# Kernel optimization log

Hardware: AMD Instinct MI355X
Metric: run time of the kernel (lower is better)

Reference implementation:

```python
import jax, jax.numpy as jnp
import numpy as np

EMB = 256
ENT_NUM = 100000
REL_NUM = 2000
B = 512


def setup_inputs() -> dict:
    key = jax.random.key(0)
    ks = jax.random.split(key, 10)
    s = 0.02
    return {
        "left_child": jax.random.normal(ks[0], (B, 3, EMB), jnp.float32),
        "right_child": jax.random.normal(ks[1], (B, 3, EMB), jnp.float32),
        "query": jax.random.normal(ks[2], (B, 3, EMB), jnp.float32),
        "ent_emb": jax.random.normal(ks[3], (ENT_NUM, EMB), jnp.float32) * s,
        "rel_emb": jax.random.normal(ks[4], (REL_NUM, EMB), jnp.float32) * s,
        "W_left": jax.random.normal(ks[5], (EMB, EMB), jnp.float32) * s,
        "b_left": jnp.zeros((EMB,), jnp.float32),
        "W_right": jax.random.normal(ks[6], (EMB, EMB), jnp.float32) * s,
        "b_right": jnp.zeros((EMB,), jnp.float32),
        "W_ent": jax.random.normal(ks[7], (EMB, 3 * EMB), jnp.float32) * s,
        "b_ent": jnp.zeros((EMB,), jnp.float32),
    }


def _attend(q, table):
    # q: [B, E], table: [N, E]. Fused form of expand*mul*sum + softmax + expand*mul*sum.
    logits = q @ table.T                     # [B, N]
    probs = jax.nn.softmax(logits, axis=1)   # [B, N]
    return probs @ table                     # [B, E]


def reference(left_child, right_child, query, ent_emb, rel_emb,
              W_left, b_left, W_right, b_right, W_ent, b_ent):
    q1 = query[:, 1, :]
    left_rel = q1 @ W_left.T + b_left
    right_rel = q1 @ W_right.T + b_right
    # cat(query[:,0], query[:,1], query[:,2]) along dim 1 == reshape
    q_cat = query.reshape(query.shape[0], 3 * EMB)
    q_ent = q_cat @ W_ent.T + b_ent

    o_ent = _attend(q_ent, ent_emb)
    o_left_r = _attend(left_rel, rel_emb)
    o_right_r = _attend(right_rel, rel_emb)

    new_left = jnp.stack([left_child[:, 0, :], o_left_r, o_ent], axis=1)
    new_right = jnp.stack([o_ent, o_right_r, right_child[:, 2, :]], axis=1)
    return (new_left, new_right)
```

## Files before the change

kernel.cpp:

```cpp
#include <hip/hip_runtime.h>
#include <hip/hip_bf16.h>
#include <math.h>

typedef __bf16 bf16;
typedef unsigned short u16;
typedef unsigned int u32;
typedef unsigned long long u64;
typedef long long i64;
typedef unsigned char u8;
typedef __attribute__((ext_vector_type(8))) __bf16 bf16x8;
typedef __attribute__((ext_vector_type(16))) float f32x16;
typedef __attribute__((ext_vector_type(8))) int i32x8;
typedef __attribute__((address_space(1))) void gvoid;
typedef __attribute__((address_space(3))) void svoid;

#define ENT_N 100000
#define REL_N 2000
#define ENT_CH 120
#define REL_CH 4

#define NPREPM 1536
#define NITEMS 6380
#define NCOPY  256

static __device__ __forceinline__ i32x8 mk8(uint4 a, uint4 b) {
    i32x8 r;
    r[0] = (int)a.x; r[1] = (int)a.y; r[2] = (int)a.z; r[3] = (int)a.w;
    r[4] = (int)b.x; r[5] = (int)b.y; r[6] = (int)b.z; r[7] = (int)b.w;
    return r;
}

template<int KLEN>
static __device__ __forceinline__ void prep_tile(
    const float* __restrict__ query, const float* __restrict__ W,
    const float* __restrict__ bias, int b0, int rowbase, int qwoff,
    bf16* __restrict__ outBf, u8* __restrict__ out8, float* smem)
{
    const int t = threadIdx.x;
    float* qs = smem;
    float* Wl = smem + 4 * KLEN;

#pragma unroll
    for (int i = 0; i < 4 * KLEN / 256; ++i) {
        const int l = t + 256 * i;
        const int r = l / KLEN, k = l % KLEN;
        qs[l] = query[(size_t)(b0 + r) * 768 + qwoff + k];
    }

    const int j = t & 63, r = t >> 6;
    const int srow = t >> 3, skq = t & 7;
    const float* wbase = W + (size_t)rowbase * KLEN;

    float4 v0, v1;
    auto wload = [&](int c) {
        v0 = *(const float4*)(wbase + (size_t)srow * KLEN + c * 32 + skq * 4);
        v1 = *(const float4*)(wbase + (size_t)(srow + 32) * KLEN + c * 32 + skq * 4);
    };
    auto wstore = [&](float* dst) {
        float* d0 = dst + srow * 33 + skq * 4;
        d0[0] = v0.x; d0[1] = v0.y; d0[2] = v0.z; d0[3] = v0.w;
        float* d1 = dst + (srow + 32) * 33 + skq * 4;
        d1[0] = v1.x; d1[1] = v1.y; d1[2] = v1.z; d1[3] = v1.w;
    };

    float acc = 0.f;
    wload(0);
    wstore(Wl);
    constexpr int NC = KLEN / 32;
    for (int c = 0; c < NC; ++c) {
        if (c + 1 < NC) wload(c + 1);
        __syncthreads();
        const float* wr = Wl + (c & 1) * 2112 + j * 33;
        const float* qr = qs + r * KLEN + c * 32;
#pragma unroll
        for (int k = 0; k < 32; ++k) acc += wr[k] * qr[k];
        if (c + 1 < NC) wstore(Wl + ((c + 1) & 1) * 2112);
    }
    acc += bias[rowbase + j];

    const size_t o = (size_t)(b0 + r) * 256 + rowbase + j;
    outBf[o] = (bf16)acc;
    out8[o] = (u8)__builtin_amdgcn_cvt_pk_fp8_f32(acc, acc, 0, false);
}

__global__ __launch_bounds__(256) void prep_conv(
    const float* __restrict__ query,
    const float* __restrict__ W_left, const float* __restrict__ b_left,
    const float* __restrict__ W_right, const float* __restrict__ b_right,
    const float* __restrict__ W_ent, const float* __restrict__ b_ent,
    const float* __restrict__ lc, const float* __restrict__ rc,
    bf16* __restrict__ qe, bf16* __restrict__ ql, bf16* __restrict__ qr,
    u8* __restrict__ qe8, u8* __restrict__ ql8, u8* __restrict__ qr8,
    float* __restrict__ out,
    const float* __restrict__ entF, const float* __restrict__ relF,
    u8* __restrict__ entT, u8* __restrict__ entB,
    u8* __restrict__ relT, u8* __restrict__ relB,
    int nconv)
{
    __shared__ float smem[7296];
    const int blk = blockIdx.x;
    const int t = threadIdx.x;

    if (blk < NPREPM) {
        const int rg = blk / 12, jt = blk % 12;
        const int b0 = rg * 4;
        const int proj = jt >> 2, rowbase = (jt & 3) * 64;
        if (proj == 0)
            prep_tile<768>(query, W_ent, b_ent, b0, rowbase, 0, qe, qe8, smem);
        else if (proj == 1)
            prep_tile<256>(query, W_left, b_left, b0, rowbase, 256, ql, ql8, smem);
        else
            prep_tile<256>(query, W_right, b_right, b0, rowbase, 256, qr, qr8, smem);
        return;
    }
    if (blk >= NPREPM + nconv) {
        const int idx = (blk - NPREPM - nconv) * 256 + t;
        if (idx < 32768) {
            const int q = idx >> 6, e4 = idx & 63;
            float4 v = *(const float4*)(lc + (size_t)q * 768 + e4 * 4);
            *(float4*)(out + (size_t)q * 768 + e4 * 4) = v;
        } else {
            const int j = idx - 32768;
            const int q = j >> 6, e4 = j & 63;
            float4 v = *(const float4*)(rc + (size_t)q * 768 + 512 + e4 * 4);
            *(float4*)(out + (size_t)393216 + q * 768 + 512 + e4 * 4) = v;
        }
        return;
    }

    const int cidx = blk - NPREPM;
    const int x = cidx >> 2, y = cidx & 3;
    const float* in; u8* outT; u8* outB; int R; int g;
    if (x < 1563) {
        in = entF; outT = entT; outB = entB; R = ENT_N; g = x;
    } else {
        in = relF; outT = relT; outB = relB; R = REL_N; g = x - 1563;
    }
    const int r0 = g * 64;
    float* tile = smem;
    const int e0 = y * 64;

    const int eg = t & 7, rowb = t >> 3;
#pragma unroll
    for (int item = 0; item < 2; ++item) {
        const int r = rowb + item * 32;
        float4 a, b;
        if ((r0 + r) < R) {
            const float* src = in + (size_t)(r0 + r) * 256 + e0 + eg * 8;
            a = *(const float4*)src;
            b = *(const float4*)(src + 4);
        } else { a = make_float4(0.f, 0.f, 0.f, 0.f); b = a; }
        float* dst = tile + r * 65 + eg * 8;
        dst[0] = a.x; dst[1] = a.y; dst[2] = a.z; dst[3] = a.w;
        dst[4] = b.x; dst[5] = b.y; dst[6] = b.z; dst[7] = b.w;
    }
    __syncthreads();

    {
        const int n2 = t >> 2, piece = t & 3;
        const int sub = n2 >> 5, nn = n2 & 31;
        const int kbk = piece >> 1, jh = piece & 1;
        const float* src = tile + n2 * 65 + kbk * 32 + jh * 16;
        u32 xx; uint4 o;
        xx = __builtin_amdgcn_cvt_pk_fp8_f32(src[0], src[1], 0, false);
        o.x = __builtin_amdgcn_cvt_pk_fp8_f32(src[2], src[3], xx, true);
        xx = __builtin_amdgcn_cvt_pk_fp8_f32(src[4], src[5], 0, false);
        o.y = __builtin_amdgcn_cvt_pk_fp8_f32(src[6], src[7], xx, true);
        xx = __builtin_amdgcn_cvt_pk_fp8_f32(src[8], src[9], 0, false);
        o.z = __builtin_amdgcn_cvt_pk_fp8_f32(src[10], src[11], xx, true);
        xx = __builtin_amdgcn_cvt_pk_fp8_f32(src[12], src[13], 0, false);
        o.w = __builtin_amdgcn_cvt_pk_fp8_f32(src[14], src[15], xx, true);
        *(uint4*)(outB + (size_t)g * 16384 + sub * 8192 +
                  (size_t)y * 2048 + kbk * 1024 + nn * 32 + jh * 16) = o;
    }
    {
        const int etl = t >> 7, kbv = (t >> 6) & 1;
        const int nv = (t >> 1) & 31, jh = t & 1;
        const int colL = etl * 32 + nv;
        float v[16];
#pragma unroll
        for (int i = 0; i < 16; ++i) {
            const int row = jh * 32 + (i & 3) + 8 * (i >> 2) + 4 * kbv;
            v[i] = tile[row * 65 + colL];
        }
        u32 xx; uint4 o;
        xx = __builtin_amdgcn_cvt_pk_fp8_f32(v[0], v[1], 0, false);
        o.x = __builtin_amdgcn_cvt_pk_fp8_f32(v[2], v[3], xx, true);
        xx = __builtin_amdgcn_cvt_pk_fp8_f32(v[4], v[5], 0, false);
        o.y = __builtin_amdgcn_cvt_pk_fp8_f32(v[6], v[7], xx, true);
        xx = __builtin_amdgcn_cvt_pk_fp8_f32(v[8], v[9], 0, false);
        o.z = __builtin_amdgcn_cvt_pk_fp8_f32(v[10], v[11], xx, true);
        xx = __builtin_amdgcn_cvt_pk_fp8_f32(v[12], v[13], 0, false);
        o.w = __builtin_amdgcn_cvt_pk_fp8_f32(v[14], v[15], xx, true);
        *(uint4*)(outT + (size_t)g * 16384 +
                  (size_t)(y * 2 + etl) * 2048 +
                  kbv * 1024 + nv * 32 + jh * 16) = o;
    }
}

__global__ __launch_bounds__(256, 2) void flash10(
    const u8* __restrict__ qeP, const u8* __restrict__ qlP,
    const u8* __restrict__ qrP,
    const u8* __restrict__ entB, const u8* __restrict__ relB,
    const u8* __restrict__ entT, const u8* __restrict__ relT,
    float* __restrict__ entL, float* __restrict__ relLL,
    float* __restrict__ relLR,
    u16* __restrict__ entO, u16* __restrict__ relOL, u16* __restrict__ relOR)
{
    const int tid = threadIdx.x;
    const int w = tid >> 6;
    const int lane = tid & 63;
    const int n = lane & 31;
    const int kb = lane >> 5;

    int qt, c, stride, nt, Nrows;
    const u8* qbf; const u8* tabB; const u8* tabT;
    float* pL; u16* pO;
    {
        const int id = blockIdx.x;
        if (id < 480) {
            qt = id / 120; c = id % 120;
            stride = 120; nt = (c < 3) ? 14 : 13;
            Nrows = ENT_N;
            qbf = qeP; tabB = entB; tabT = entT; pL = entL; pO = entO;
        } else {
            const int r = id - 480;
            qt = (r >> 2) & 3; c = r & 3;
            stride = 4; nt = 8;
            Nrows = REL_N;
            tabB = relB; tabT = relT;
            if (r < 16) { qbf = qlP; pL = relLL; pO = relOL; }
            else        { qbf = qrP; pL = relLR; pO = relOR; }
        }
    }
    const int q0 = qt * 128;
    const int qw = q0 + w * 32;

    __shared__ __align__(16) u8 lds[65536];
    u16* lds16 = (u16*)lds;

    const u8* qrow = qbf + (size_t)(qw + n) * 256;
    i32x8 qf[4];
#pragma unroll
    for (int kc = 0; kc < 4; ++kc) {
        uint4 a = *(const uint4*)(qrow + kc * 64 + kb * 32);
        uint4 b = *(const uint4*)(qrow + kc * 64 + kb * 32 + 16);
        qf[kc] = mk8(a, b);
    }

    f32x16 acc[8];
#pragma unroll
    for (int et = 0; et < 8; ++et)
#pragma unroll
        for (int i = 0; i < 16; ++i) acc[et][i] = 0.f;
    float l_run = 0.f;

    auto stage = [&](int buf, int g) {
        u8* sK = lds + buf * 32768;
        u8* sV = sK + 16384;
        const u8* ksrc = tabB + (size_t)g * 16384 + w * 4096 + (size_t)lane * 16;
        const u8* vsrc = tabT + (size_t)g * 16384 + w * 4096 + (size_t)lane * 16;
#pragma unroll
        for (int o = 0; o < 4096; o += 1024) {
            __builtin_amdgcn_global_load_lds((gvoid*)(ksrc + o),
                                             (svoid*)(sK + w * 4096 + o), 16, 0, 0);
            __builtin_amdgcn_global_load_lds((gvoid*)(vsrc + o),
                                             (svoid*)(sV + w * 4096 + o), 16, 0, 0);
        }
    };

    int rt = c;
    stage(0, rt);
    __syncthreads();

    for (int k = 0; k < nt; ++k) {
        if (k + 1 < nt) stage((k + 1) & 1, rt + stride);

        const u8* sK = lds + (k & 1) * 32768;
        const u8* sV = sK + 16384;
        const int gr = rt * 64;

        f32x16 L0, L1;
#pragma unroll
        for (int i = 0; i < 16; ++i) { L0[i] = 0.f; L1[i] = 0.f; }
        const u8* kbase = sK + kb * 1024 + n * 32;
#pragma unroll
        for (int kc = 0; kc < 4; ++kc) {
            uint4 a0 = *(const uint4*)(kbase + kc * 2048);
            uint4 a1 = *(const uint4*)(kbase + kc * 2048 + 16);
            L0 = __builtin_amdgcn_mfma_scale_f32_32x32x64_f8f6f4(
                mk8(a0, a1), qf[kc], L0, 0, 0, 0, 0x7f7f7f7f, 0, 0x7f7f7f7f);
            uint4 b0 = *(const uint4*)(kbase + 8192 + kc * 2048);
            uint4 b1 = *(const uint4*)(kbase + 8192 + kc * 2048 + 16);
            L1 = __builtin_amdgcn_mfma_scale_f32_32x32x64_f8f6f4(
                mk8(b0, b1), qf[kc], L1, 0, 0, 0, 0x7f7f7f7f, 0, 0x7f7f7f7f);
        }
        if (gr + 64 > Nrows) {
#pragma unroll
            for (int r = 0; r < 16; ++r) {
                const int row = (r & 3) + 8 * (r >> 2) + 4 * kb;
                if (gr + row >= Nrows)      L0[r] = -1e30f;
                if (gr + 32 + row >= Nrows) L1[r] = -1e30f;
            }
        }
        float rs = 0.f;
#pragma unroll
        for (int r = 0; r < 16; ++r) {
            const float p0 = __expf(L0[r]); L0[r] = p0; rs += p0;
            const float p1 = __expf(L1[r]); L1[r] = p1; rs += p1;
        }
        rs += __shfl_xor(rs, 32);
        l_run += rs;
        u32 p[8];
#pragma unroll
        for (int i = 0; i < 4; ++i) {
            u32 x = __builtin_amdgcn_cvt_pk_fp8_f32(L0[i * 4 + 0], L0[i * 4 + 1], 0, false);
            p[i] = __builtin_amdgcn_cvt_pk_fp8_f32(L0[i * 4 + 2], L0[i * 4 + 3], x, true);
            u32 y = __builtin_amdgcn_cvt_pk_fp8_f32(L1[i * 4 + 0], L1[i * 4 + 1], 0, false);
            p[i + 4] = __builtin_amdgcn_cvt_pk_fp8_f32(L1[i * 4 + 2], L1[i * 4 + 3], y, true);
        }
        uint4 pa; pa.x = p[0]; pa.y = p[1]; pa.z = p[2]; pa.w = p[3];
        uint4 pb; pb.x = p[4]; pb.y = p[5]; pb.z = p[6]; pb.w = p[7];
        const i32x8 bv = mk8(pa, pb);
        const u8* vbase = sV + kb * 1024 + n * 32;
#pragma unroll
        for (int et = 0; et < 8; ++et) {
            uint4 v0 = *(const uint4*)(vbase + et * 2048);
            uint4 v1 = *(const uint4*)(vbase + et * 2048 + 16);
            acc[et] = __builtin_amdgcn_mfma_scale_f32_32x32x64_f8f6f4(
                mk8(v0, v1), bv, acc[et], 0, 0, 0, 0x7f7f7f7f, 0, 0x7f7f7f7f);
        }
        rt += stride;
        __syncthreads();
    }

    if (lane < 32) pL[(size_t)c * 512 + qw + n] = l_run;

    for (int half = 0; half < 2; ++half) {
        __syncthreads();
        if ((w >> 1) == half) {
            u16* rgn = lds16 + (w & 1) * 8448;
#pragma unroll
            for (int et = 0; et < 8; ++et)
#pragma unroll
                for (int a2 = 0; a2 < 4; ++a2) {
                    bf16 h0 = (bf16)acc[et][a2 * 4 + 0];
                    bf16 h1 = (bf16)acc[et][a2 * 4 + 1];
                    bf16 h2 = (bf16)acc[et][a2 * 4 + 2];
                    bf16 h3 = (bf16)acc[et][a2 * 4 + 3];
                    uint2 pk;
                    pk.x = ((u32)(*(u16*)&h1) << 16) | (u32)(*(u16*)&h0);
                    pk.y = ((u32)(*(u16*)&h3) << 16) | (u32)(*(u16*)&h2);
                    *(uint2*)(rgn + n * 264 + et * 32 + 8 * a2 + 4 * kb) = pk;
                }
        }
        __syncthreads();
#pragma unroll
        for (int rg = 0; rg < 2; ++rg) {
            const int qt2 = q0 + (half * 2 + rg) * 32;
            const u16* src = lds16 + rg * 8448;
            const int qq = tid >> 3, e0 = (tid & 7) * 32;
#pragma unroll
            for (int i = 0; i < 4; ++i) {
                const u16* sp = src + qq * 264 + e0 + i * 8;
                uint2 a = *(const uint2*)(sp);
                uint2 b = *(const uint2*)(sp + 4);
                uint4 wv; wv.x = a.x; wv.y = a.y; wv.z = b.x; wv.w = b.y;
                *(uint4*)(pO + ((size_t)c * 512 + qt2 + qq) * 256 + e0 + i * 8) = wv;
            }
        }
    }
}

__global__ __launch_bounds__(256) void combine_all(
    const u16* __restrict__ entO, const float* __restrict__ entL,
    const u16* __restrict__ relOL, const float* __restrict__ relLL,
    const u16* __restrict__ relOR, const float* __restrict__ relLR,
    float* __restrict__ out)
{
    const u16* pO; const float* pl; int CH, baseA, baseB;
    if (blockIdx.y == 0) { pO = entO; pl = entL; CH = ENT_CH; baseA = 512; baseB = 393216; }
    else if (blockIdx.y == 1) { pO = relOL; pl = relLL; CH = REL_CH; baseA = 256; baseB = -1; }
    else { pO = relOR; pl = relLR; CH = REL_CH; baseA = 393472; baseB = -1; }

    const int t = threadIdx.x;
    const int qi = t >> 7;
    const int e0g = (t >> 2) & 31;
    const int seg = t & 3;
    const int q = blockIdx.x * 2 + qi;
    const int e0 = e0g * 8;
    const int cnt = CH >> 2;
    const int cbeg = seg * cnt;

    float s = 0.f;
    float a[8];
#pragma unroll
    for (int k = 0; k < 8; ++k) a[k] = 0.f;
#pragma unroll 6
    for (int c = cbeg; c < cbeg + cnt; ++c) {
        s += pl[(size_t)c * 512 + q];
        const uint4 wv = *(const uint4*)(pO + ((size_t)c * 512 + q) * 256 + e0);
        const u32 ww[4] = {wv.x, wv.y, wv.z, wv.w};
#pragma unroll
        for (int p = 0; p < 4; ++p) {
            a[p * 2]     += __uint_as_float((ww[p] & 0xffffu) << 16);
            a[p * 2 + 1] += __uint_as_float(ww[p] & 0xffff0000u);
        }
    }

    __shared__ float red[2][32][4][11];
    float* slot = red[qi][e0g][seg];
#pragma unroll
    for (int k = 0; k < 8; ++k) slot[k] = a[k];
    slot[8] = s;
    __syncthreads();
    if (seg == 0) {
        float st = 0.f;
        float b[8];
#pragma unroll
        for (int k = 0; k < 8; ++k) b[k] = 0.f;
#pragma unroll
        for (int sgi = 0; sgi < 4; ++sgi) {
            const float* sl = red[qi][e0g][sgi];
            st += sl[8];
#pragma unroll
            for (int k = 0; k < 8; ++k) b[k] += sl[k];
        }
        const float inv = 1.f / st;
#pragma unroll
        for (int k = 0; k < 8; ++k) b[k] *= inv;
        float4 o1 = {b[0], b[1], b[2], b[3]};
        float4 o2 = {b[4], b[5], b[6], b[7]};
        *(float4*)(out + (size_t)baseA + (size_t)q * 768 + e0) = o1;
        *(float4*)(out + (size_t)baseA + (size_t)q * 768 + e0 + 4) = o2;
        if (baseB >= 0) {
            *(float4*)(out + (size_t)baseB + (size_t)q * 768 + e0) = o1;
            *(float4*)(out + (size_t)baseB + (size_t)q * 768 + e0 + 4) = o2;
        }
    }
}

__global__ __launch_bounds__(256) void attend_simple(
    const bf16* __restrict__ qbf, const float* __restrict__ tab, int Nrows,
    float* __restrict__ out, int baseA, int baseB)
{
    const int q = blockIdx.x;
    const int t = threadIdx.x, wave = t >> 6, lane = t & 63;
    float qv[4];
#pragma unroll
    for (int i = 0; i < 4; ++i) qv[i] = (float)qbf[(size_t)q * 256 + lane + 64 * i];
    float m = -INFINITY, l = 0.f, o[4] = {0.f, 0.f, 0.f, 0.f};
    for (int r = wave; r < Nrows; r += 4) {
        const float* row = tab + (size_t)r * 256;
        float d = 0.f;
#pragma unroll
        for (int i = 0; i < 4; ++i) d += qv[i] * row[lane + 64 * i];
#pragma unroll
        for (int s = 32; s; s >>= 1) d += __shfl_xor(d, s);
        const float mn = fmaxf(m, d);
        const float al = __expf(m - mn);
        const float p = __expf(d - mn);
#pragma unroll
        for (int i = 0; i < 4; ++i) o[i] = o[i] * al + p * row[lane + 64 * i];
        l = l * al + p; m = mn;
    }
    __shared__ float sm[4], sl[4], so[4][256];
    if (lane == 0) { sm[wave] = m; sl[wave] = l; }
#pragma unroll
    for (int i = 0; i < 4; ++i) so[wave][lane + 64 * i] = o[i];
    __syncthreads();
    const float M = fmaxf(fmaxf(sm[0], sm[1]), fmaxf(sm[2], sm[3]));
    const float w0 = __expf(sm[0] - M), w1 = __expf(sm[1] - M);
    const float w2 = __expf(sm[2] - M), w3 = __expf(sm[3] - M);
    const float L = w0 * sl[0] + w1 * sl[1] + w2 * sl[2] + w3 * sl[3];
    const float a = (w0 * so[0][t] + w1 * so[1][t] + w2 * so[2][t] + w3 * so[3][t]) / L;
    out[(size_t)baseA + (size_t)q * 768 + t] = a;
    if (baseB >= 0) out[(size_t)baseB + (size_t)q * 768 + t] = a;
}

extern "C" void kernel_launch(void* const* d_in, const int* in_sizes, int n_in,
                              void* d_out, int out_size, void* d_ws, size_t ws_size,
                              hipStream_t stream)
{
    const float* left_child  = (const float*)d_in[0];
    const float* right_child = (const float*)d_in[1];
    const float* query       = (const float*)d_in[2];
    const float* ent_emb     = (const float*)d_in[3];
    const float* rel_emb     = (const float*)d_in[4];
    const float* W_left      = (const float*)d_in[5];
    const float* b_left      = (const float*)d_in[6];
    const float* W_right     = (const float*)d_in[7];
    const float* b_right     = (const float*)d_in[8];
    const float* W_ent       = (const float*)d_in[9];
    const float* b_ent       = (const float*)d_in[10];
    float* out = (float*)d_out;
    char* ws = (char*)d_ws;

    bf16* qe_bf = (bf16*)(ws + 0);
    bf16* ql_bf = (bf16*)(ws + 262144);
    bf16* qr_bf = (bf16*)(ws + 524288);
    u8*   qe8   = (u8*)(ws + 786432);
    u8*   ql8   = (u8*)(ws + 917504);
    u8*   qr8   = (u8*)(ws + 1048576);
    u8*   entT8 = (u8*)(ws + 1179648);
    u8*   relT8 = (u8*)(ws + 26787840);
    u8*   entB8 = (u8*)(ws + 27312128);
    u8*   relB8 = (u8*)(ws + 52920320);
    float* entL = (float*)(ws + 53444608);
    u16*  entO  = (u16*)(ws + 53690368);
    float* relLL = (float*)(ws + 85147648);
    float* relLR = (float*)(ws + 85155840);
    u16*  relOL = (u16*)(ws + 85164032);
    u16*  relOR = (u16*)(ws + 86212608);
    const size_t WS_FULL = 87261184;
    const size_t WS_FALLBACK = 786432;

    if (ws_size >= WS_FULL) {
        prep_conv<<<dim3(NPREPM + NITEMS + NCOPY), dim3(256), 0, stream>>>(
            query, W_left, b_left, W_right, b_right, W_ent, b_ent,
            left_child, right_child, qe_bf, ql_bf, qr_bf, qe8, ql8, qr8, out,
            ent_emb, rel_emb, entT8, entB8, relT8, relB8, NITEMS);
        flash10<<<dim3(512), dim3(256), 0, stream>>>(
            qe8, ql8, qr8, entB8, relB8, entT8, relT8,
            entL, relLL, relLR, entO, relOL, relOR);
        combine_all<<<dim3(256, 3), dim3(256), 0, stream>>>(
            entO, entL, relOL, relLL, relOR, relLR, out);
    } else if (ws_size >= WS_FALLBACK) {
        prep_conv<<<dim3(NPREPM + NCOPY), dim3(256), 0, stream>>>(
            query, W_left, b_left, W_right, b_right, W_ent, b_ent,
            left_child, right_child, qe_bf, ql_bf, qr_bf, qe8, ql8, qr8, out,
            ent_emb, rel_emb, (u8*)ws, (u8*)ws, (u8*)ws, (u8*)ws, 0);
        attend_simple<<<dim3(512), dim3(256), 0, stream>>>(qe_bf, ent_emb, ENT_N, out, 512, 393216);
        attend_simple<<<dim3(512), dim3(256), 0, stream>>>(ql_bf, rel_emb, REL_N, out, 256, -1);
        attend_simple<<<dim3(512), dim3(256), 0, stream>>>(qr_bf, rel_emb, REL_N, out, 393472, -1);
    }
    (void)in_sizes; (void)n_in; (void)out_size;
}
```

Before: 236.8 us.

## Coarsen fp8 conversion blocks to process four column slices with prefetch

Each conversion block now handles all four 64-column slices of a 64-row group instead of one, prefetching the next slice's global loads into registers while the current slice is converted and stored. The copy blocks each move four float4 items per thread instead of one. This cuts the grid from ~8k to ~3.2k blocks and overlaps load latency with the conversion work. In exchange it adds extra barriers per block and reduces parallelism per block count.

```diff
diff --git a/kernel.cpp b/kernel.cpp
--- a/kernel.cpp
+++ b/kernel.cpp
@@ -8,7 +8,6 @@
 typedef unsigned long long u64;
 typedef long long i64;
 typedef unsigned char u8;
-typedef __attribute__((ext_vector_type(8))) __bf16 bf16x8;
 typedef __attribute__((ext_vector_type(16))) float f32x16;
 typedef __attribute__((ext_vector_type(8))) int i32x8;
 typedef __attribute__((address_space(1))) void gvoid;
@@ -20,8 +19,8 @@
 #define REL_CH 4
 
 #define NPREPM 1536
-#define NITEMS 6380
-#define NCOPY  256
+#define NCONVG 1595
+#define NCOPYB 64
 
 static __device__ __forceinline__ i32x8 mk8(uint4 a, uint4 b) {
     i32x8 r;
@@ -114,87 +113,101 @@
         return;
     }
     if (blk >= NPREPM + nconv) {
-        const int idx = (blk - NPREPM - nconv) * 256 + t;
-        if (idx < 32768) {
-            const int q = idx >> 6, e4 = idx & 63;
-            float4 v = *(const float4*)(lc + (size_t)q * 768 + e4 * 4);
-            *(float4*)(out + (size_t)q * 768 + e4 * 4) = v;
-        } else {
-            const int j = idx - 32768;
-            const int q = j >> 6, e4 = j & 63;
-            float4 v = *(const float4*)(rc + (size_t)q * 768 + 512 + e4 * 4);
-            *(float4*)(out + (size_t)393216 + q * 768 + 512 + e4 * 4) = v;
+        const int base = (blk - NPREPM - nconv) * 256 + t;
+#pragma unroll
+        for (int i = 0; i < 4; ++i) {
+            const int idx = base + i * 16384;
+            if (idx < 32768) {
+                const int q = idx >> 6, e4 = idx & 63;
+                float4 v = *(const float4*)(lc + (size_t)q * 768 + e4 * 4);
+                *(float4*)(out + (size_t)q * 768 + e4 * 4) = v;
+            } else {
+                const int j = idx - 32768;
+                const int q = j >> 6, e4 = j & 63;
+                float4 v = *(const float4*)(rc + (size_t)q * 768 + 512 + e4 * 4);
+                *(float4*)(out + (size_t)393216 + q * 768 + 512 + e4 * 4) = v;
+            }
         }
         return;
     }
 
-    const int cidx = blk - NPREPM;
-    const int x = cidx >> 2, y = cidx & 3;
+    const int cb = blk - NPREPM;
     const float* in; u8* outT; u8* outB; int R; int g;
-    if (x < 1563) {
-        in = entF; outT = entT; outB = entB; R = ENT_N; g = x;
+    if (cb < 1563) {
+        in = entF; outT = entT; outB = entB; R = ENT_N; g = cb;
     } else {
-        in = relF; outT = relT; outB = relB; R = REL_N; g = x - 1563;
+        in = relF; outT = relT; outB = relB; R = REL_N; g = cb - 1563;
     }
     const int r0 = g * 64;
     float* tile = smem;
-    const int e0 = y * 64;
-
     const int eg = t & 7, rowb = t >> 3;
-#pragma unroll
-    for (int item = 0; item < 2; ++item) {
-        const int r = rowb + item * 32;
-        float4 a, b;
-        if ((r0 + r) < R) {
-            const float* src = in + (size_t)(r0 + r) * 256 + e0 + eg * 8;
-            a = *(const float4*)src;
-            b = *(const float4*)(src + 4);
-        } else { a = make_float4(0.f, 0.f, 0.f, 0.f); b = a; }
-        float* dst = tile + r * 65 + eg * 8;
-        dst[0] = a.x; dst[1] = a.y; dst[2] = a.z; dst[3] = a.w;
-        dst[4] = b.x; dst[5] = b.y; dst[6] = b.z; dst[7] = b.w;
-    }
-    __syncthreads();
-
-    {
-        const int n2 = t >> 2, piece = t & 3;
-        const int sub = n2 >> 5, nn = n2 & 31;
-        const int kbk = piece >> 1, jh = piece & 1;
-        const float* src = tile + n2 * 65 + kbk * 32 + jh * 16;
-        u32 xx; uint4 o;
-        xx = __builtin_amdgcn_cvt_pk_fp8_f32(src[0], src[1], 0, false);
-        o.x = __builtin_amdgcn_cvt_pk_fp8_f32(src[2], src[3], xx, true);
-        xx = __builtin_amdgcn_cvt_pk_fp8_f32(src[4], src[5], 0, false);
-        o.y = __builtin_amdgcn_cvt_pk_fp8_f32(src[6], src[7], xx, true);
-        xx = __builtin_amdgcn_cvt_pk_fp8_f32(src[8], src[9], 0, false);
-        o.z = __builtin_amdgcn_cvt_pk_fp8_f32(src[10], src[11], xx, true);
-        xx = __builtin_amdgcn_cvt_pk_fp8_f32(src[12], src[13], 0, false);
-        o.w = __builtin_amdgcn_cvt_pk_fp8_f32(src[14], src[15], xx, true);
-        *(uint4*)(outB + (size_t)g * 16384 + sub * 8192 +
-                  (size_t)y * 2048 + kbk * 1024 + nn * 32 + jh * 16) = o;
-    }
-    {
-        const int etl = t >> 7, kbv = (t >> 6) & 1;
-        const int nv = (t >> 1) & 31, jh = t & 1;
-        const int colL = etl * 32 + nv;
-        float v[16];
-#pragma unroll
-        for (int i = 0; i < 16; ++i) {
-            const int row = jh * 32 + (i & 3) + 8 * (i >> 2) + 4 * kbv;
-            v[i] = tile[row * 65 + colL];
-        }
-        u32 xx; uint4 o;
-        xx = __builtin_amdgcn_cvt_pk_fp8_f32(v[0], v[1], 0, false);
-        o.x = __builtin_amdgcn_cvt_pk_fp8_f32(v[2], v[3], xx, true);
-        xx = __builtin_amdgcn_cvt_pk_fp8_f32(v[4], v[5], 0, false);
-        o.y = __builtin_amdgcn_cvt_pk_fp8_f32(v[6], v[7], xx, true);
-        xx = __builtin_amdgcn_cvt_pk_fp8_f32(v[8], v[9], 0, false);
-        o.z = __builtin_amdgcn_cvt_pk_fp8_f32(v[10], v[11], xx, true);
-        xx = __builtin_amdgcn_cvt_pk_fp8_f32(v[12], v[13], 0, false);
-        o.w = __builtin_amdgcn_cvt_pk_fp8_f32(v[14], v[15], xx, true);
-        *(uint4*)(outT + (size_t)g * 16384 +
-                  (size_t)(y * 2 + etl) * 2048 +
-                  kbv * 1024 + nv * 32 + jh * 16) = o;
+    const bool vA = (r0 + rowb) < R, vB = (r0 + rowb + 32) < R;
+    const float* rowA = in + (size_t)(r0 + rowb) * 256 + eg * 8;
+    const float* rowB = in + (size_t)(r0 + rowb + 32) * 256 + eg * 8;
+
+    float4 A0, B0, A1, B1;
+    auto cissue = [&](int y) {
+        const int e0 = y * 64;
+        if (vA) { A0 = *(const float4*)(rowA + e0); B0 = *(const float4*)(rowA + e0 + 4); }
+        else    { A0 = make_float4(0.f, 0.f, 0.f, 0.f); B0 = A0; }
+        if (vB) { A1 = *(const float4*)(rowB + e0); B1 = *(const float4*)(rowB + e0 + 4); }
+        else    { A1 = make_float4(0.f, 0.f, 0.f, 0.f); B1 = A1; }
+    };
+
+    cissue(0);
+#pragma unroll
+    for (int y = 0; y < 4; ++y) {
+        __syncthreads();
+        {
+            float* d0 = tile + rowb * 65 + eg * 8;
+            d0[0] = A0.x; d0[1] = A0.y; d0[2] = A0.z; d0[3] = A0.w;
+            d0[4] = B0.x; d0[5] = B0.y; d0[6] = B0.z; d0[7] = B0.w;
+            float* d1 = tile + (rowb + 32) * 65 + eg * 8;
+            d1[0] = A1.x; d1[1] = A1.y; d1[2] = A1.z; d1[3] = A1.w;
+            d1[4] = B1.x; d1[5] = B1.y; d1[6] = B1.z; d1[7] = B1.w;
+        }
+        if (y + 1 < 4) cissue(y + 1);
+        __syncthreads();
+        {
+            const int n2 = t >> 2, piece = t & 3;
+            const int sub = n2 >> 5, nn = n2 & 31;
+            const int kbk = piece >> 1, jh = piece & 1;
+            const float* src = tile + n2 * 65 + kbk * 32 + jh * 16;
+            u32 xx; uint4 o;
+            xx = __builtin_amdgcn_cvt_pk_fp8_f32(src[0], src[1], 0, false);
+            o.x = __builtin_amdgcn_cvt_pk_fp8_f32(src[2], src[3], xx, true);
+            xx = __builtin_amdgcn_cvt_pk_fp8_f32(src[4], src[5], 0, false);
+            o.y = __builtin_amdgcn_cvt_pk_fp8_f32(src[6], src[7], xx, true);
+            xx = __builtin_amdgcn_cvt_pk_fp8_f32(src[8], src[9], 0, false);
+            o.z = __builtin_amdgcn_cvt_pk_fp8_f32(src[10], src[11], xx, true);
+            xx = __builtin_amdgcn_cvt_pk_fp8_f32(src[12], src[13], 0, false);
+            o.w = __builtin_amdgcn_cvt_pk_fp8_f32(src[14], src[15], xx, true);
+            *(uint4*)(outB + (size_t)g * 16384 + sub * 8192 +
+                      (size_t)y * 2048 + kbk * 1024 + nn * 32 + jh * 16) = o;
+        }
+        {
+            const int etl = t >> 7, kbv = (t >> 6) & 1;
+            const int nv = (t >> 1) & 31, jh = t & 1;
+            const int colL = etl * 32 + nv;
+            float v[16];
+#pragma unroll
+            for (int i = 0; i < 16; ++i) {
+                const int row = jh * 32 + (i & 3) + 8 * (i >> 2) + 4 * kbv;
+                v[i] = tile[row * 65 + colL];
+            }
+            u32 xx; uint4 o;
+            xx = __builtin_amdgcn_cvt_pk_fp8_f32(v[0], v[1], 0, false);
+            o.x = __builtin_amdgcn_cvt_pk_fp8_f32(v[2], v[3], xx, true);
+            xx = __builtin_amdgcn_cvt_pk_fp8_f32(v[4], v[5], 0, false);
+            o.y = __builtin_amdgcn_cvt_pk_fp8_f32(v[6], v[7], xx, true);
+            xx = __builtin_amdgcn_cvt_pk_fp8_f32(v[8], v[9], 0, false);
+            o.z = __builtin_amdgcn_cvt_pk_fp8_f32(v[10], v[11], xx, true);
+            xx = __builtin_amdgcn_cvt_pk_fp8_f32(v[12], v[13], 0, false);
+            o.w = __builtin_amdgcn_cvt_pk_fp8_f32(v[14], v[15], xx, true);
+            *(uint4*)(outT + (size_t)g * 16384 +
+                      (size_t)(y * 2 + etl) * 2048 +
+                      kbv * 1024 + nv * 32 + jh * 16) = o;
+        }
     }
 }
 
@@ -516,17 +529,17 @@
     const size_t WS_FALLBACK = 786432;
 
     if (ws_size >= WS_FULL) {
-        prep_conv<<<dim3(NPREPM + NITEMS + NCOPY), dim3(256), 0, stream>>>(
+        prep_conv<<<dim3(NPREPM + NCONVG + NCOPYB), dim3(256), 0, stream>>>(
             query, W_left, b_left, W_right, b_right, W_ent, b_ent,
             left_child, right_child, qe_bf, ql_bf, qr_bf, qe8, ql8, qr8, out,
-            ent_emb, rel_emb, entT8, entB8, relT8, relB8, NITEMS);
+            ent_emb, rel_emb, entT8, entB8, relT8, relB8, NCONVG);
         flash10<<<dim3(512), dim3(256), 0, stream>>>(
             qe8, ql8, qr8, entB8, relB8, entT8, relT8,
             entL, relLL, relLR, entO, relOL, relOR);
         combine_all<<<dim3(256, 3), dim3(256), 0, stream>>>(
             entO, entL, relOL, relLL, relOR, relLR, out);
     } else if (ws_size >= WS_FALLBACK) {
-        prep_conv<<<dim3(NPREPM + NCOPY), dim3(256), 0, stream>>>(
+        prep_conv<<<dim3(NPREPM + NCOPYB), dim3(256), 0, stream>>>(
             query, W_left, b_left, W_right, b_right, W_ent, b_ent,
             left_child, right_child, qe_bf, ql_bf, qr_bf, qe8, ql8, qr8, out,
             ent_emb, rel_emb, (u8*)ws, (u8*)ws, (u8*)ws, (u8*)ws, 0);
```

New measurement: 238.4 us. Within noise of the previous version (+0.7%).

## Fuse flash attention and combine kernels via software grid barrier

Applied to the files above, without the earlier changes.

Merges the flash-attention partial kernel and the combine kernel into one launch, separated by an atomic-counter grid barrier, with a memset added to reset the counter each call. This removes one kernel launch and the gap between kernels. It relies on all 512 blocks being co-resident (256 CUs at 2 blocks per CU) or the barrier deadlocks, and it adds a memset plus spin-wait overhead. The combine work is now spread over 512 blocks in a grid-stride loop instead of 768 blocks.

```diff
diff --git a/kernel.cpp b/kernel.cpp
--- a/kernel.cpp
+++ b/kernel.cpp
@@ -8,7 +8,6 @@
 typedef unsigned long long u64;
 typedef long long i64;
 typedef unsigned char u8;
-typedef __attribute__((ext_vector_type(8))) __bf16 bf16x8;
 typedef __attribute__((ext_vector_type(16))) float f32x16;
 typedef __attribute__((ext_vector_type(8))) int i32x8;
 typedef __attribute__((address_space(1))) void gvoid;
@@ -22,12 +21,25 @@
 #define NPREPM 1536
 #define NITEMS 6380
 #define NCOPY  256
+#define NBLK   512
 
 static __device__ __forceinline__ i32x8 mk8(uint4 a, uint4 b) {
     i32x8 r;
     r[0] = (int)a.x; r[1] = (int)a.y; r[2] = (int)a.z; r[3] = (int)a.w;
     r[4] = (int)b.x; r[5] = (int)b.y; r[6] = (int)b.z; r[7] = (int)b.w;
     return r;
+}
+
+static __device__ __forceinline__ void grid_barrier(u32* cnt) {
+    __syncthreads();
+    if (threadIdx.x == 0) {
+        __threadfence();
+        atomicAdd(cnt, 1u);
+        while (atomicAdd(cnt, 0u) < (u32)NBLK)
+            __builtin_amdgcn_s_sleep(2);
+        __threadfence();
+    }
+    __syncthreads();
 }
 
 template<int KLEN>
@@ -198,14 +210,15 @@
     }
 }
 
-__global__ __launch_bounds__(256, 2) void flash10(
+__global__ __launch_bounds__(256, 2) void flash_combine(
     const u8* __restrict__ qeP, const u8* __restrict__ qlP,
     const u8* __restrict__ qrP,
     const u8* __restrict__ entB, const u8* __restrict__ relB,
     const u8* __restrict__ entT, const u8* __restrict__ relT,
     float* __restrict__ entL, float* __restrict__ relLL,
     float* __restrict__ relLR,
-    u16* __restrict__ entO, u16* __restrict__ relOL, u16* __restrict__ relOR)
+    u16* __restrict__ entO, u16* __restrict__ relOL, u16* __restrict__ relOR,
+    float* __restrict__ out, u32* __restrict__ cnt0)
 {
     const int tid = threadIdx.x;
     const int w = tid >> 6;
@@ -213,229 +226,232 @@
     const int n = lane & 31;
     const int kb = lane >> 5;
 
-    int qt, c, stride, nt, Nrows;
-    const u8* qbf; const u8* tabB; const u8* tabT;
-    float* pL; u16* pO;
-    {
-        const int id = blockIdx.x;
-        if (id < 480) {
-            qt = id / 120; c = id % 120;
-            stride = 120; nt = (c < 3) ? 14 : 13;
-            Nrows = ENT_N;
-            qbf = qeP; tabB = entB; tabT = entT; pL = entL; pO = entO;
-        } else {
-            const int r = id - 480;
-            qt = (r >> 2) & 3; c = r & 3;
-            stride = 4; nt = 8;
-            Nrows = REL_N;
-            tabB = relB; tabT = relT;
-            if (r < 16) { qbf = qlP; pL = relLL; pO = relOL; }
-            else        { qbf = qrP; pL = relLR; pO = relOR; }
-        }
-    }
-    const int q0 = qt * 128;
-    const int qw = q0 + w * 32;
-
     __shared__ __align__(16) u8 lds[65536];
     u16* lds16 = (u16*)lds;
 
-    const u8* qrow = qbf + (size_t)(qw + n) * 256;
-    i32x8 qf[4];
-#pragma unroll
-    for (int kc = 0; kc < 4; ++kc) {
-        uint4 a = *(const uint4*)(qrow + kc * 64 + kb * 32);
-        uint4 b = *(const uint4*)(qrow + kc * 64 + kb * 32 + 16);
-        qf[kc] = mk8(a, b);
-    }
-
-    f32x16 acc[8];
-#pragma unroll
-    for (int et = 0; et < 8; ++et)
-#pragma unroll
-        for (int i = 0; i < 16; ++i) acc[et][i] = 0.f;
-    float l_run = 0.f;
-
-    auto stage = [&](int buf, int g) {
-        u8* sK = lds + buf * 32768;
-        u8* sV = sK + 16384;
-        const u8* ksrc = tabB + (size_t)g * 16384 + w * 4096 + (size_t)lane * 16;
-        const u8* vsrc = tabT + (size_t)g * 16384 + w * 4096 + (size_t)lane * 16;
-#pragma unroll
-        for (int o = 0; o < 4096; o += 1024) {
-            __builtin_amdgcn_global_load_lds((gvoid*)(ksrc + o),
-                                             (svoid*)(sK + w * 4096 + o), 16, 0, 0);
-            __builtin_amdgcn_global_load_lds((gvoid*)(vsrc + o),
-                                             (svoid*)(sV + w * 4096 + o), 16, 0, 0);
-        }
-    };
-
-    int rt = c;
-    stage(0, rt);
-    __syncthreads();
-
-    for (int k = 0; k < nt; ++k) {
-        if (k + 1 < nt) stage((k + 1) & 1, rt + stride);
-
-        const u8* sK = lds + (k & 1) * 32768;
-        const u8* sV = sK + 16384;
-        const int gr = rt * 64;
-
-        f32x16 L0, L1;
-#pragma unroll
-        for (int i = 0; i < 16; ++i) { L0[i] = 0.f; L1[i] = 0.f; }
-        const u8* kbase = sK + kb * 1024 + n * 32;
+    {
+        int qt, c, stride, nt, Nrows;
+        const u8* qbf; const u8* tabB; const u8* tabT;
+        float* pL; u16* pO;
+        {
+            const int id = blockIdx.x;
+            if (id < 480) {
+                qt = id / 120; c = id % 120;
+                stride = 120; nt = (c < 3) ? 14 : 13;
+                Nrows = ENT_N;
+                qbf = qeP; tabB = entB; tabT = entT; pL = entL; pO = entO;
+            } else {
+                const int r = id - 480;
+                qt = (r >> 2) & 3; c = r & 3;
+                stride = 4; nt = 8;
+                Nrows = REL_N;
+                tabB = relB; tabT = relT;
+                if (r < 16) { qbf = qlP; pL = relLL; pO = relOL; }
+                else        { qbf = qrP; pL = relLR; pO = relOR; }
+            }
+        }
+        const int q0 = qt * 128;
+        const int qw = q0 + w * 32;
+
+        const u8* qrow = qbf + (size_t)(qw + n) * 256;
+        i32x8 qf[4];
 #pragma unroll
         for (int kc = 0; kc < 4; ++kc) {
-            uint4 a0 = *(const uint4*)(kbase + kc * 2048);
-            uint4 a1 = *(const uint4*)(kbase + kc * 2048 + 16);
-            L0 = __builtin_amdgcn_mfma_scale_f32_32x32x64_f8f6f4(
-                mk8(a0, a1), qf[kc], L0, 0, 0, 0, 0x7f7f7f7f, 0, 0x7f7f7f7f);
-            uint4 b0 = *(const uint4*)(kbase + 8192 + kc * 2048);
-            uint4 b1 = *(const uint4*)(kbase + 8192 + kc * 2048 + 16);
-            L1 = __builtin_amdgcn_mfma_scale_f32_32x32x64_f8f6f4(
-                mk8(b0, b1), qf[kc], L1, 0, 0, 0, 0x7f7f7f7f, 0, 0x7f7f7f7f);
-        }
-        if (gr + 64 > Nrows) {
+            uint4 a = *(const uint4*)(qrow + kc * 64 + kb * 32);
+            uint4 b = *(const uint4*)(qrow + kc * 64 + kb * 32 + 16);
+            qf[kc] = mk8(a, b);
+        }
+
+        f32x16 acc[8];
+#pragma unroll
+        for (int et = 0; et < 8; ++et)
+#pragma unroll
+            for (int i = 0; i < 16; ++i) acc[et][i] = 0.f;
+        float l_run = 0.f;
+
+        auto stage = [&](int buf, int g) {
+            u8* sK = lds + buf * 32768;
+            u8* sV = sK + 16384;
+            const u8* ksrc = tabB + (size_t)g * 16384 + w * 4096 + (size_t)lane * 16;
+            const u8* vsrc = tabT + (size_t)g * 16384 + w * 4096 + (size_t)lane * 16;
+#pragma unroll
+            for (int o = 0; o < 4096; o += 1024) {
+                __builtin_amdgcn_global_load_lds((gvoid*)(ksrc + o),
+                                                 (svoid*)(sK + w * 4096 + o), 16, 0, 0);
+                __builtin_amdgcn_global_load_lds((gvoid*)(vsrc + o),
+                                                 (svoid*)(sV + w * 4096 + o), 16, 0, 0);
+            }
+        };
+
+        int rt = c;
+        stage(0, rt);
+        __syncthreads();
+
+        for (int k = 0; k < nt; ++k) {
+            if (k + 1 < nt) stage((k + 1) & 1, rt + stride);
+
+            const u8* sK = lds + (k & 1) * 32768;
+            const u8* sV = sK + 16384;
+            const int gr = rt * 64;
+
+            f32x16 L0, L1;
+#pragma unroll
+            for (int i = 0; i < 16; ++i) { L0[i] = 0.f; L1[i] = 0.f; }
+            const u8* kbase = sK + kb * 1024 + n * 32;
+#pragma unroll
+            for (int kc = 0; kc < 4; ++kc) {
+                uint4 a0 = *(const uint4*)(kbase + kc * 2048);
+                uint4 a1 = *(const uint4*)(kbase + kc * 2048 + 16);
+                L0 = __builtin_amdgcn_mfma_scale_f32_32x32x64_f8f6f4(
+                    mk8(a0, a1), qf[kc], L0, 0, 0, 0, 0x7f7f7f7f, 0, 0x7f7f7f7f);
+                uint4 b0 = *(const uint4*)(kbase + 8192 + kc * 2048);
+                uint4 b1 = *(const uint4*)(kbase + 8192 + kc * 2048 + 16);
+                L1 = __builtin_amdgcn_mfma_scale_f32_32x32x64_f8f6f4(
+                    mk8(b0, b1), qf[kc], L1, 0, 0, 0, 0x7f7f7f7f, 0, 0x7f7f7f7f);
+            }
+            if (gr + 64 > Nrows) {
+#pragma unroll
+                for (int r = 0; r < 16; ++r) {
+                    const int row = (r & 3) + 8 * (r >> 2) + 4 * kb;
+                    if (gr + row >= Nrows)      L0[r] = -1e30f;
+                    if (gr + 32 + row >= Nrows) L1[r] = -1e30f;
+                }
+            }
+            float rs = 0.f;
 #pragma unroll
             for (int r = 0; r < 16; ++r) {
-                const int row = (r & 3) + 8 * (r >> 2) + 4 * kb;
-                if (gr + row >= Nrows)      L0[r] = -1e30f;
-                if (gr + 32 + row >= Nrows) L1[r] = -1e30f;
-            }
-        }
-        float rs = 0.f;
-#pragma unroll
-        for (int r = 0; r < 16; ++r) {
-            const float p0 = __expf(L0[r]); L0[r] = p0; rs += p0;
-            const float p1 = __expf(L1[r]); L1[r] = p1; rs += p1;
-        }
-        rs += __shfl_xor(rs, 32);
-        l_run += rs;
-        u32 p[8];
-#pragma unroll
-        for (int i = 0; i < 4; ++i) {
-            u32 x = __builtin_amdgcn_cvt_pk_fp8_f32(L0[i * 4 + 0], L0[i * 4 + 1], 0, false);
-            p[i] = __builtin_amdgcn_cvt_pk_fp8_f32(L0[i * 4 + 2], L0[i * 4 + 3], x, true);
-            u32 y = __builtin_amdgcn_cvt_pk_fp8_f32(L1[i * 4 + 0], L1[i * 4 + 1], 0, false);
-            p[i + 4] = __builtin_amdgcn_cvt_pk_fp8_f32(L1[i * 4 + 2], L1[i * 4 + 3], y, true);
-        }
-        uint4 pa; pa.x = p[0]; pa.y = p[1]; pa.z = p[2]; pa.w = p[3];
-        uint4 pb; pb.x = p[4]; pb.y = p[5]; pb.z = p[6]; pb.w = p[7];
-        const i32x8 bv = mk8(pa, pb);
-        const u8* vbase = sV + kb * 1024 + n * 32;
-#pragma unroll
-        for (int et = 0; et < 8; ++et) {
-            uint4 v0 = *(const uint4*)(vbase + et * 2048);
-            uint4 v1 = *(const uint4*)(vbase + et * 2048 + 16);
-            acc[et] = __builtin_amdgcn_mfma_scale_f32_32x32x64_f8f6f4(
-                mk8(v0, v1), bv, acc[et], 0, 0, 0, 0x7f7f7f7f, 0, 0x7f7f7f7f);
-        }
-        rt += stride;
-        __syncthreads();
-    }
-
-    if (lane < 32) pL[(size_t)c * 512 + qw + n] = l_run;
-
-    for (int half = 0; half < 2; ++half) {
-        __syncthreads();
-        if ((w >> 1) == half) {
-            u16* rgn = lds16 + (w & 1) * 8448;
-#pragma unroll
-            for (int et = 0; et < 8; ++et)
-#pragma unroll
-                for (int a2 = 0; a2 < 4; ++a2) {
-                    bf16 h0 = (bf16)acc[et][a2 * 4 + 0];
-                    bf16 h1 = (bf16)acc[et][a2 * 4 + 1];
-                    bf16 h2 = (bf16)acc[et][a2 * 4 + 2];
-                    bf16 h3 = (bf16)acc[et][a2 * 4 + 3];
-                    uint2 pk;
-                    pk.x = ((u32)(*(u16*)&h1) << 16) | (u32)(*(u16*)&h0);
-                    pk.y = ((u32)(*(u16*)&h3) << 16) | (u32)(*(u16*)&h2);
-                    *(uint2*)(rgn + n * 264 + et * 32 + 8 * a2 + 4 * kb) = pk;
+                const float p0 = __expf(L0[r]); L0[r] = p0; rs += p0;
+                const float p1 = __expf(L1[r]); L1[r] = p1; rs += p1;
+            }
+            rs += __shfl_xor(rs, 32);
+            l_run += rs;
+            u32 p[8];
+#pragma unroll
+            for (int i = 0; i < 4; ++i) {
+                u32 x = __builtin_amdgcn_cvt_pk_fp8_f32(L0[i * 4 + 0], L0[i * 4 + 1], 0, false);
+                p[i] = __builtin_amdgcn_cvt_pk_fp8_f32(L0[i * 4 + 2], L0[i * 4 + 3], x, true);
+                u32 y = __builtin_amdgcn_cvt_pk_fp8_f32(L1[i * 4 + 0], L1[i * 4 + 1], 0, false);
+                p[i + 4] = __builtin_amdgcn_cvt_pk_fp8_f32(L1[i * 4 + 2], L1[i * 4 + 3], y, true);
+            }
+            uint4 pa; pa.x = p[0]; pa.y = p[1]; pa.z = p[2]; pa.w = p[3];
+            uint4 pb; pb.x = p[4]; pb.y = p[5]; pb.z = p[6]; pb.w = p[7];
+            const i32x8 bv = mk8(pa, pb);
+            const u8* vbase = sV + kb * 1024 + n * 32;
+#pragma unroll
+            for (int et = 0; et < 8; ++et) {
+                uint4 v0 = *(const uint4*)(vbase + et * 2048);
+                uint4 v1 = *(const uint4*)(vbase + et * 2048 + 16);
+                acc[et] = __builtin_amdgcn_mfma_scale_f32_32x32x64_f8f6f4(
+                    mk8(v0, v1), bv, acc[et], 0, 0, 0, 0x7f7f7f7f, 0, 0x7f7f7f7f);
+            }
+            rt += stride;
+            __syncthreads();
+        }
+
+        if (lane < 32) pL[(size_t)c * 512 + qw + n] = l_run;
+
+        for (int half = 0; half < 2; ++half) {
+            __syncthreads();
+            if ((w >> 1) == half) {
+                u16* rgn = lds16 + (w & 1) * 8448;
+#pragma unroll
+                for (int et = 0; et < 8; ++et)
+#pragma unroll
+                    for (int a2 = 0; a2 < 4; ++a2) {
+                        bf16 h0 = (bf16)acc[et][a2 * 4 + 0];
+                        bf16 h1 = (bf16)acc[et][a2 * 4 + 1];
+                        bf16 h2 = (bf16)acc[et][a2 * 4 + 2];
+                        bf16 h3 = (bf16)acc[et][a2 * 4 + 3];
+                        uint2 pk;
+                        pk.x = ((u32)(*(u16*)&h1) << 16) | (u32)(*(u16*)&h0);
+                        pk.y = ((u32)(*(u16*)&h3) << 16) | (u32)(*(u16*)&h2);
+                        *(uint2*)(rgn + n * 264 + et * 32 + 8 * a2 + 4 * kb) = pk;
+                    }
+            }
+            __syncthreads();
+#pragma unroll
+            for (int rg = 0; rg < 2; ++rg) {
+                const int qt2 = q0 + (half * 2 + rg) * 32;
+                const u16* src = lds16 + rg * 8448;
+                const int qq = tid >> 3, e0 = (tid & 7) * 32;
+#pragma unroll
+                for (int i = 0; i < 4; ++i) {
+                    const u16* sp = src + qq * 264 + e0 + i * 8;
+                    uint2 a = *(const uint2*)(sp);
+                    uint2 b = *(const uint2*)(sp + 4);
+                    uint4 wv; wv.x = a.x; wv.y = a.y; wv.z = b.x; wv.w = b.y;
+                    *(uint4*)(pO + ((size_t)c * 512 + qt2 + qq) * 256 + e0 + i * 8) = wv;
                 }
-        }
-        __syncthreads();
-#pragma unroll
-        for (int rg = 0; rg < 2; ++rg) {
-            const int qt2 = q0 + (half * 2 + rg) * 32;
-            const u16* src = lds16 + rg * 8448;
-            const int qq = tid >> 3, e0 = (tid & 7) * 32;
-#pragma unroll
-            for (int i = 0; i < 4; ++i) {
-                const u16* sp = src + qq * 264 + e0 + i * 8;
-                uint2 a = *(const uint2*)(sp);
-                uint2 b = *(const uint2*)(sp + 4);
-                uint4 wv; wv.x = a.x; wv.y = a.y; wv.z = b.x; wv.w = b.y;
-                *(uint4*)(pO + ((size_t)c * 512 + qt2 + qq) * 256 + e0 + i * 8) = wv;
-            }
-        }
-    }
-}
-
-__global__ __launch_bounds__(256) void combine_all(
-    const u16* __restrict__ entO, const float* __restrict__ entL,
-    const u16* __restrict__ relOL, const float* __restrict__ relLL,
-    const u16* __restrict__ relOR, const float* __restrict__ relLR,
-    float* __restrict__ out)
-{
-    const u16* pO; const float* pl; int CH, baseA, baseB;
-    if (blockIdx.y == 0) { pO = entO; pl = entL; CH = ENT_CH; baseA = 512; baseB = 393216; }
-    else if (blockIdx.y == 1) { pO = relOL; pl = relLL; CH = REL_CH; baseA = 256; baseB = -1; }
-    else { pO = relOR; pl = relLR; CH = REL_CH; baseA = 393472; baseB = -1; }
-
-    const int t = threadIdx.x;
-    const int qi = t >> 7;
-    const int e0g = (t >> 2) & 31;
-    const int seg = t & 3;
-    const int q = blockIdx.x * 2 + qi;
-    const int e0 = e0g * 8;
-    const int cnt = CH >> 2;
-    const int cbeg = seg * cnt;
-
-    float s = 0.f;
-    float a[8];
-#pragma unroll
-    for (int k = 0; k < 8; ++k) a[k] = 0.f;
+            }
+        }
+    }
+    grid_barrier(cnt0);
+
+    {
+        const int t = threadIdx.x;
+        typedef float RedT[32][4][11];
+        RedT* red = (RedT*)lds;
+        for (int v = blockIdx.x; v < 768; v += NBLK) {
+            __syncthreads();
+            const int gx = v & 255, gy = v >> 8;
+            const u16* pO; const float* pl; int CH, baseA, baseB;
+            if (gy == 0) { pO = entO; pl = entL; CH = ENT_CH; baseA = 512; baseB = 393216; }
+            else if (gy == 1) { pO = relOL; pl = relLL; CH = REL_CH; baseA = 256; baseB = -1; }
+            else { pO = relOR; pl = relLR; CH = REL_CH; baseA = 393472; baseB = -1; }
+
+            const int qi = t >> 7;
+            const int e0g = (t >> 2) & 31;
+            const int seg = t & 3;
+            const int q = gx * 2 + qi;
+            const int e0 = e0g * 8;
+            const int cnt = CH >> 2;
+            const int cbeg = seg * cnt;
+
+            float s = 0.f;
+            float a[8];
+#pragma unroll
+            for (int k = 0; k < 8; ++k) a[k] = 0.f;
 #pragma unroll 6
-    for (int c = cbeg; c < cbeg + cnt; ++c) {
-        s += pl[(size_t)c * 512 + q];
-        const uint4 wv = *(const uint4*)(pO + ((size_t)c * 512 + q) * 256 + e0);
-        const u32 ww[4] = {wv.x, wv.y, wv.z, wv.w};
-#pragma unroll
-        for (int p = 0; p < 4; ++p) {
-            a[p * 2]     += __uint_as_float((ww[p] & 0xffffu) << 16);
-            a[p * 2 + 1] += __uint_as_float(ww[p] & 0xffff0000u);
-        }
-    }
-
-    __shared__ float red[2][32][4][11];
-    float* slot = red[qi][e0g][seg];
-#pragma unroll
-    for (int k = 0; k < 8; ++k) slot[k] = a[k];
-    slot[8] = s;
-    __syncthreads();
-    if (seg == 0) {
-        float st = 0.f;
-        float b[8];
-#pragma unroll
-        for (int k = 0; k < 8; ++k) b[k] = 0.f;
-#pragma unroll
-        for (int sgi = 0; sgi < 4; ++sgi) {
-            const float* sl = red[qi][e0g][sgi];
-            st += sl[8];
-#pragma unroll
-            for (int k = 0; k < 8; ++k) b[k] += sl[k];
-        }
-        const float inv = 1.f / st;
-#pragma unroll
-        for (int k = 0; k < 8; ++k) b[k] *= inv;
-        float4 o1 = {b[0], b[1], b[2], b[3]};
-        float4 o2 = {b[4], b[5], b[6], b[7]};
-        *(float4*)(out + (size_t)baseA + (size_t)q * 768 + e0) = o1;
-        *(float4*)(out + (size_t)baseA + (size_t)q * 768 + e0 + 4) = o2;
-        if (baseB >= 0) {
-            *(float4*)(out + (size_t)baseB + (size_t)q * 768 + e0) = o1;
-            *(float4*)(out + (size_t)baseB + (size_t)q * 768 + e0 + 4) = o2;
+            for (int c = cbeg; c < cbeg + cnt; ++c) {
+                s += pl[(size_t)c * 512 + q];
+                const uint4 wv = *(const uint4*)(pO + ((size_t)c * 512 + q) * 256 + e0);
+                const u32 ww[4] = {wv.x, wv.y, wv.z, wv.w};
+#pragma unroll
+                for (int p = 0; p < 4; ++p) {
+                    a[p * 2]     += __uint_as_float((ww[p] & 0xffffu) << 16);
+                    a[p * 2 + 1] += __uint_as_float(ww[p] & 0xffff0000u);
+                }
+            }
+
+            float* slot = red[qi][e0g][seg];
+#pragma unroll
+            for (int k = 0; k < 8; ++k) slot[k] = a[k];
+            slot[8] = s;
+            __syncthreads();
+            if (seg == 0) {
+                float st = 0.f;
+                float b[8];
+#pragma unroll
+                for (int k = 0; k < 8; ++k) b[k] = 0.f;
+#pragma unroll
+                for (int sgi = 0; sgi < 4; ++sgi) {
+                    const float* sl = red[qi][e0g][sgi];
+                    st += sl[8];
+#pragma unroll
+                    for (int k = 0; k < 8; ++k) b[k] += sl[k];
+                }
+                const float inv = 1.f / st;
+#pragma unroll
+                for (int k = 0; k < 8; ++k) b[k] *= inv;
+                float4 o1 = {b[0], b[1], b[2], b[3]};
+                float4 o2 = {b[4], b[5], b[6], b[7]};
+                *(float4*)(out + (size_t)baseA + (size_t)q * 768 + e0) = o1;
+                *(float4*)(out + (size_t)baseA + (size_t)q * 768 + e0 + 4) = o2;
+                if (baseB >= 0) {
+                    *(float4*)(out + (size_t)baseB + (size_t)q * 768 + e0) = o1;
+                    *(float4*)(out + (size_t)baseB + (size_t)q * 768 + e0 + 4) = o2;
+                }
+            }
         }
     }
 }
@@ -512,19 +528,19 @@
     float* relLR = (float*)(ws + 85155840);
     u16*  relOL = (u16*)(ws + 85164032);
     u16*  relOR = (u16*)(ws + 86212608);
-    const size_t WS_FULL = 87261184;
+    u32*  cnts  = (u32*)(ws + 87261184);
+    const size_t WS_FULL = 87261440;
     const size_t WS_FALLBACK = 786432;
 
     if (ws_size >= WS_FULL) {
+        hipMemsetAsync((void*)cnts, 0, 256, stream);
         prep_conv<<<dim3(NPREPM + NITEMS + NCOPY), dim3(256), 0, stream>>>(
             query, W_left, b_left, W_right, b_right, W_ent, b_ent,
             left_child, right_child, qe_bf, ql_bf, qr_bf, qe8, ql8, qr8, out,
             ent_emb, rel_emb, entT8, entB8, relT8, relB8, NITEMS);
-        flash10<<<dim3(512), dim3(256), 0, stream>>>(
+        flash_combine<<<dim3(NBLK), dim3(256), 0, stream>>>(
             qe8, ql8, qr8, entB8, relB8, entT8, relT8,
-            entL, relLL, relLR, entO, relOL, relOR);
-        combine_all<<<dim3(256, 3), dim3(256), 0, stream>>>(
-            entO, entL, relOL, relLL, relOR, relLR, out);
+            entL, relLL, relLR, entO, relOL, relOR, out, cnts);
     } else if (ws_size >= WS_FALLBACK) {
         prep_conv<<<dim3(NPREPM + NCOPY), dim3(256), 0, stream>>>(
             query, W_left, b_left, W_right, b_right, W_ent, b_ent,
```

Result: slower. 318.4 us (+34.5%).

## Load K/V fp8 tiles directly from global memory instead of LDS double buffering

Applied to the files above, without the earlier changes.

Removes the async global-to-LDS double-buffered staging of key and value tiles and the per-iteration barrier. Each wave now reads its MFMA operands straight from global memory (relying on L2 and the cache), and shared memory shrinks to the epilogue buffer, so more blocks can be resident per CU. The cost is that all four waves re-fetch the same K/V tile from global memory, four times the load traffic, and the prefetch overlap is lost.

```diff
diff --git a/kernel.cpp b/kernel.cpp
--- a/kernel.cpp
+++ b/kernel.cpp
@@ -8,7 +8,6 @@
 typedef unsigned long long u64;
 typedef long long i64;
 typedef unsigned char u8;
-typedef __attribute__((ext_vector_type(8))) __bf16 bf16x8;
 typedef __attribute__((ext_vector_type(16))) float f32x16;
 typedef __attribute__((ext_vector_type(8))) int i32x8;
 typedef __attribute__((address_space(1))) void gvoid;
@@ -198,7 +197,7 @@
     }
 }
 
-__global__ __launch_bounds__(256, 2) void flash10(
+__global__ __launch_bounds__(256) void flash11(
     const u8* __restrict__ qeP, const u8* __restrict__ qlP,
     const u8* __restrict__ qrP,
     const u8* __restrict__ entB, const u8* __restrict__ relB,
@@ -236,8 +235,7 @@
     const int q0 = qt * 128;
     const int qw = q0 + w * 32;
 
-    __shared__ __align__(16) u8 lds[65536];
-    u16* lds16 = (u16*)lds;
+    __shared__ __align__(16) u16 lds16[16896];
 
     const u8* qrow = qbf + (size_t)(qw + n) * 256;
     i32x8 qf[4];
@@ -255,43 +253,23 @@
         for (int i = 0; i < 16; ++i) acc[et][i] = 0.f;
     float l_run = 0.f;
 
-    auto stage = [&](int buf, int g) {
-        u8* sK = lds + buf * 32768;
-        u8* sV = sK + 16384;
-        const u8* ksrc = tabB + (size_t)g * 16384 + w * 4096 + (size_t)lane * 16;
-        const u8* vsrc = tabT + (size_t)g * 16384 + w * 4096 + (size_t)lane * 16;
-#pragma unroll
-        for (int o = 0; o < 4096; o += 1024) {
-            __builtin_amdgcn_global_load_lds((gvoid*)(ksrc + o),
-                                             (svoid*)(sK + w * 4096 + o), 16, 0, 0);
-            __builtin_amdgcn_global_load_lds((gvoid*)(vsrc + o),
-                                             (svoid*)(sV + w * 4096 + o), 16, 0, 0);
-        }
-    };
-
     int rt = c;
-    stage(0, rt);
-    __syncthreads();
-
     for (int k = 0; k < nt; ++k) {
-        if (k + 1 < nt) stage((k + 1) & 1, rt + stride);
-
-        const u8* sK = lds + (k & 1) * 32768;
-        const u8* sV = sK + 16384;
+        const u8* kbB = tabB + (size_t)rt * 16384 + kb * 1024 + n * 32;
+        const u8* vbB = tabT + (size_t)rt * 16384 + kb * 1024 + n * 32;
         const int gr = rt * 64;
 
         f32x16 L0, L1;
 #pragma unroll
         for (int i = 0; i < 16; ++i) { L0[i] = 0.f; L1[i] = 0.f; }
-        const u8* kbase = sK + kb * 1024 + n * 32;
 #pragma unroll
         for (int kc = 0; kc < 4; ++kc) {
-            uint4 a0 = *(const uint4*)(kbase + kc * 2048);
-            uint4 a1 = *(const uint4*)(kbase + kc * 2048 + 16);
+            uint4 a0 = *(const uint4*)(kbB + kc * 2048);
+            uint4 a1 = *(const uint4*)(kbB + kc * 2048 + 16);
             L0 = __builtin_amdgcn_mfma_scale_f32_32x32x64_f8f6f4(
                 mk8(a0, a1), qf[kc], L0, 0, 0, 0, 0x7f7f7f7f, 0, 0x7f7f7f7f);
-            uint4 b0 = *(const uint4*)(kbase + 8192 + kc * 2048);
-            uint4 b1 = *(const uint4*)(kbase + 8192 + kc * 2048 + 16);
+            uint4 b0 = *(const uint4*)(kbB + 8192 + kc * 2048);
+            uint4 b1 = *(const uint4*)(kbB + 8192 + kc * 2048 + 16);
             L1 = __builtin_amdgcn_mfma_scale_f32_32x32x64_f8f6f4(
                 mk8(b0, b1), qf[kc], L1, 0, 0, 0, 0x7f7f7f7f, 0, 0x7f7f7f7f);
         }
@@ -322,16 +300,14 @@
         uint4 pa; pa.x = p[0]; pa.y = p[1]; pa.z = p[2]; pa.w = p[3];
         uint4 pb; pb.x = p[4]; pb.y = p[5]; pb.z = p[6]; pb.w = p[7];
         const i32x8 bv = mk8(pa, pb);
-        const u8* vbase = sV + kb * 1024 + n * 32;
 #pragma unroll
         for (int et = 0; et < 8; ++et) {
-            uint4 v0 = *(const uint4*)(vbase + et * 2048);
-            uint4 v1 = *(const uint4*)(vbase + et * 2048 + 16);
+            uint4 v0 = *(const uint4*)(vbB + et * 2048);
+            uint4 v1 = *(const uint4*)(vbB + et * 2048 + 16);
             acc[et] = __builtin_amdgcn_mfma_scale_f32_32x32x64_f8f6f4(
                 mk8(v0, v1), bv, acc[et], 0, 0, 0, 0x7f7f7f7f, 0, 0x7f7f7f7f);
         }
         rt += stride;
-        __syncthreads();
     }
 
     if (lane < 32) pL[(size_t)c * 512 + qw + n] = l_run;
@@ -520,7 +496,7 @@
             query, W_left, b_left, W_right, b_right, W_ent, b_ent,
             left_child, right_child, qe_bf, ql_bf, qr_bf, qe8, ql8, qr8, out,
             ent_emb, rel_emb, entT8, entB8, relT8, relB8, NITEMS);
-        flash10<<<dim3(512), dim3(256), 0, stream>>>(
+        flash11<<<dim3(512), dim3(256), 0, stream>>>(
             qe8, ql8, qr8, entB8, relB8, entT8, relT8,
             entL, relLL, relLR, entO, relOL, relOR);
         combine_all<<<dim3(256, 3), dim3(256), 0, stream>>>(
```

After: 254.1 us. +7.3%, slower.
